# Kernel optimization log

Hardware: AMD Instinct MI355X
Metric: run time of the kernel (lower is better)

## Reference

```python
import jax, jax.numpy as jnp
import numpy as np

N, F_IN, HID, H1, E = 50000, 512, 128, 4, 800000
NEG_SLOPE = 0.2

def setup_inputs() -> dict:
    key = jax.random.key(0)
    ks = jax.random.split(key, 10)
    s = lambda fan: 1.0 / np.sqrt(fan)
    x = jax.random.normal(ks[0], (N, F_IN), jnp.float32)
    edge_index = jax.random.randint(ks[1], (2, E), 0, N, jnp.int32)
    W1 = jax.random.normal(ks[2], (F_IN, H1 * HID), jnp.float32) * s(F_IN)
    a_src1 = jax.random.normal(ks[3], (H1, HID), jnp.float32) * s(HID)
    a_dst1 = jax.random.normal(ks[4], (H1, HID), jnp.float32) * s(HID)
    b1 = jnp.zeros((H1 * HID,), jnp.float32)
    W2 = jax.random.normal(ks[5], (H1 * HID, HID), jnp.float32) * s(H1 * HID)
    a_src2 = jax.random.normal(ks[6], (1, HID), jnp.float32) * s(HID)
    a_dst2 = jax.random.normal(ks[7], (1, HID), jnp.float32) * s(HID)
    b2 = jnp.zeros((HID,), jnp.float32)
    return {"x": x, "edge_index": edge_index, "W1": W1, "a_src1": a_src1,
            "a_dst1": a_dst1, "b1": b1, "W2": W2, "a_src2": a_src2,
            "a_dst2": a_dst2, "b2": b2}

def _gat(x, src, dst, W, a_src, a_dst, b, n):
    H, C = a_src.shape
    h = (x @ W).reshape(-1, H, C)                      # [N, H, C]
    # per-edge attention logits: alpha_src[src] + alpha_dst[dst]
    e = jax.nn.leaky_relu((h * a_src).sum(-1)[src] + (h * a_dst).sum(-1)[dst],
                          NEG_SLOPE)                   # [E', H]
    # segment softmax over destination node
    m = jax.ops.segment_max(e, dst, num_segments=n)
    p = jnp.exp(e - m[dst])
    denom = jax.ops.segment_sum(p, dst, num_segments=n)
    alpha = p / (denom[dst] + 1e-16)
    # weighted scatter-add aggregation
    out = jax.ops.segment_sum(h[src] * alpha[:, :, None], dst, num_segments=n)
    return out.reshape(-1, H * C) + b

def reference(x, edge_index, W1, a_src1, a_dst1, b1, W2, a_src2, a_dst2, b2):
    loops = jnp.arange(N, dtype=edge_index.dtype)      # add_self_loops=True
    src = jnp.concatenate([edge_index[0], loops])
    dst = jnp.concatenate([edge_index[1], loops])
    h = jax.nn.elu(_gat(x, src, dst, W1, a_src1, a_dst1, b1, N))
    return _gat(h, src, dst, W2, a_src2, a_dst2, b2, N)
```

## Files before the change

kernel.cpp:

```cpp
#include <hip/hip_runtime.h>
#include <hip/hip_bf16.h>
#include <math.h>

#define NEG_SLOPE 0.2f

constexpr int N_NODES = 50000;
constexpr int F_IN    = 512;
constexpr int HID     = 128;
constexpr int H1      = 4;
constexpr int E_EDGES = 800000;
constexpr int E_TOT   = E_EDGES + N_NODES;
constexpr int DEG_CAP = 64;

typedef __attribute__((ext_vector_type(8))) short short8;
typedef __attribute__((ext_vector_type(4))) float floatx4;
typedef __attribute__((ext_vector_type(2))) float f32x2;
typedef __attribute__((ext_vector_type(4))) unsigned short ushort4v;

__device__ __forceinline__ unsigned short f2bf(float f) {
  union { float f; unsigned int u; } v; v.f = f;
  unsigned int u = v.u + 0x7FFFu + ((v.u >> 16) & 1u);
  return (unsigned short)(u >> 16);
}
__device__ __forceinline__ float bf_lo(unsigned int u) {
  union { unsigned int u; float f; } v; v.u = u << 16; return v.f;
}
__device__ __forceinline__ float bf_hi(unsigned int u) {
  union { unsigned int u; float f; } v; v.u = u & 0xFFFF0000u; return v.f;
}

__device__ __forceinline__ void store_val(float* p, float v) { *p = v; }
__device__ __forceinline__ void store_val(unsigned short* p, float v) { *p = f2bf(v); }

template <int CPT>
__device__ __forceinline__ void store_vec(unsigned short* p, const float* v) {
#pragma unroll
  for (int c = 0; c < CPT; c += 4) {
    ushort4v o;
#pragma unroll
    for (int j = 0; j < 4; ++j) o[j] = f2bf(v[c + j]);
    *(ushort4v*)(p + c) = o;
  }
}
template <int CPT>
__device__ __forceinline__ void store_vec(float* p, const float* v) {
#pragma unroll
  for (int c = 0; c < CPT; c += 4) *(float4*)(p + c) = *(const float4*)(v + c);
}

__device__ __forceinline__ void async_load16(const void* g, void* lds) {
  __builtin_amdgcn_global_load_lds(
      (const __attribute__((address_space(1))) unsigned int*)g,
      (__attribute__((address_space(3))) unsigned int*)lds, 16, 0, 0);
}

__global__ void prep_kernel(const float* __restrict__ W1, const float* __restrict__ W2,
                            unsigned short* __restrict__ W1t, unsigned short* __restrict__ W2t,
                            int* __restrict__ cnt) {
  int i = blockIdx.x * 256 + threadIdx.x;
  if (i < N_NODES) cnt[i] = 0;
  int j = i - N_NODES;
  if (j >= 0 && j < 512 * 512) {
    int n = j >> 9, k = j & 511;
    W1t[j] = f2bf(W1[k * 512 + n]);
  }
  int l = i - N_NODES - 512 * 512;
  if (l >= 0 && l < 128 * 512) {
    int n = l >> 9, k = l & 511;
    W2t[l] = f2bf(W2[k * 128 + n]);
  }
}

__global__ void fill_kernel(const int* __restrict__ ei, int* __restrict__ cnt,
                            int* __restrict__ adj) {
  int i = blockIdx.x * blockDim.x + threadIdx.x;
  if (i >= E_TOT) return;
  int s, d;
  if (i < E_EDGES) { s = ei[i]; d = ei[E_EDGES + i]; }
  else             { s = i - E_EDGES; d = s; }
  int pos = atomicAdd(&cnt[d], 1);
  if (pos < DEG_CAP) adj[d * DEG_CAP + pos] = s;
}

template <bool CVT_A, typename OT>
__global__ __launch_bounds__(256) void gemm_bf16_kernel(
    const void* __restrict__ Araw, const unsigned short* __restrict__ Bt,
    OT* __restrict__ C, const float* __restrict__ a_srcp, const float* __restrict__ a_dstp,
    float* __restrict__ alpha_src, float* __restrict__ alpha_dst,
    int M, int N, int K, int Hn, int nRowTiles) {
  __shared__ unsigned short As[128 * 32];
  __shared__ unsigned short Bs[128 * 32];
  __shared__ float red_s[128][2];
  __shared__ float red_d[128][2];

  int grp = blockIdx.x / (8 * Hn);
  int w8 = blockIdx.x % (8 * Hn);
  int head = w8 >> 3;
  int rowTile = grp * 8 + (w8 & 7);
  if (rowTile >= nRowTiles) return;
  int row0 = rowTile * 128;
  int col0 = head * 128;

  int tid = threadIdx.x;
  int lane = tid & 63, wave = tid >> 6;
  int wm = wave & 1, wn = wave >> 1;
  int l15 = lane & 15, quad = lane >> 4;

  floatx4 acc[4][4];
#pragma unroll
  for (int i = 0; i < 4; ++i)
#pragma unroll
    for (int j = 0; j < 4; ++j) acc[i][j] = (floatx4){0.f, 0.f, 0.f, 0.f};

  int seg_b = wave * 2;
  int r_in = (lane >> 2);
  int c8 = (lane & 3) * 8;

  for (int k0 = 0; k0 < K; k0 += 32) {
#pragma unroll
    for (int p = 0; p < 2; ++p) {
      int seg = seg_b + p;
      int r = seg * 16 + r_in;
      int gc = col0 + r;
      async_load16(Bt + (size_t)gc * K + k0 + c8, &Bs[seg * 512]);
    }
    if constexpr (CVT_A) {
      const float* Af = (const float*)Araw;
#pragma unroll
      for (int p = 0; p < 4; ++p) {
        int lin = tid + p * 256;
        int r = lin >> 3;
        int q = lin & 7;
        int gr = row0 + r; if (gr >= M) gr = M - 1;
        float4 f = *(const float4*)(Af + (size_t)gr * K + k0 + q * 4);
        ushort4v o;
        o[0] = f2bf(f.x); o[1] = f2bf(f.y); o[2] = f2bf(f.z); o[3] = f2bf(f.w);
        *(ushort4v*)&As[r * 32 + q * 4] = o;
      }
    } else {
      const unsigned short* Ab = (const unsigned short*)Araw;
#pragma unroll
      for (int p = 0; p < 2; ++p) {
        int seg = seg_b + p;
        int r = seg * 16 + r_in;
        int gr = row0 + r; if (gr >= M) gr = M - 1;
        async_load16(Ab + (size_t)gr * K + k0 + c8, &As[seg * 512]);
      }
    }
    __syncthreads();

    short8 a[4], b[4];
#pragma unroll
    for (int mi = 0; mi < 4; ++mi)
      a[mi] = *(const short8*)&As[(wm * 64 + mi * 16 + l15) * 32 + quad * 8];
#pragma unroll
    for (int ni = 0; ni < 4; ++ni)
      b[ni] = *(const short8*)&Bs[(wn * 64 + ni * 16 + l15) * 32 + quad * 8];
#pragma unroll
    for (int mi = 0; mi < 4; ++mi)
#pragma unroll
      for (int ni = 0; ni < 4; ++ni)
        acc[mi][ni] = __builtin_amdgcn_mfma_f32_16x16x32_bf16(a[mi], b[ni], acc[mi][ni], 0, 0, 0);
    __syncthreads();
  }

  float a_s[4], a_d[4];
#pragma unroll
  for (int ni = 0; ni < 4; ++ni) {
    int cih = wn * 64 + ni * 16 + l15;
    a_s[ni] = a_srcp[head * HID + cih];
    a_d[ni] = a_dstp[head * HID + cih];
  }

#pragma unroll
  for (int mi = 0; mi < 4; ++mi) {
#pragma unroll
    for (int r = 0; r < 4; ++r) {
      int rloc = wm * 64 + mi * 16 + quad * 4 + r;
      int grow = row0 + rloc;
      float ps = 0.f, pd = 0.f;
#pragma unroll
      for (int ni = 0; ni < 4; ++ni) {
        float v = acc[mi][ni][r];
        ps += v * a_s[ni];
        pd += v * a_d[ni];
        if (grow < M) {
          int gcol = col0 + wn * 64 + ni * 16 + l15;
          store_val(&C[(size_t)grow * N + gcol], v);
        }
      }
#pragma unroll
      for (int off = 1; off < 16; off <<= 1) {
        ps += __shfl_xor(ps, off);
        pd += __shfl_xor(pd, off);
      }
      if (l15 == 0) { red_s[rloc][wn] = ps; red_d[rloc][wn] = pd; }
    }
  }
  __syncthreads();
  if (tid < 128) {
    int grow = row0 + tid;
    if (grow < M) {
      alpha_src[(size_t)grow * Hn + head] = red_s[tid][0] + red_s[tid][1];
      alpha_dst[(size_t)grow * Hn + head] = red_d[tid][0] + red_d[tid][1];
    }
  }
}

template <int H, typename OT>
__global__ __launch_bounds__(256) void aggregate_kernel(
    const unsigned short* __restrict__ h, const float* __restrict__ asrc,
    const float* __restrict__ adst, const int* __restrict__ cnt,
    const int* __restrict__ adj, const float* __restrict__ bias,
    OT* __restrict__ out, int apply_elu, int nNodes) {
  constexpr int CPT = 8;
  constexpr int CH = H * HID;
  constexpr int NCH = CH / CPT;
  constexpr int SLOTS = 64 / NCH;
  constexpr int NW = 4;
  __shared__ float p_sh[NW][64 * H];
  __shared__ int ro_sh[NW][64];

  const int wv = threadIdx.x >> 6;
  const int lane = threadIdx.x & 63;
  const int node = blockIdx.x * NW + wv;
  if (node >= nNodes) return;
  int deg = cnt[node];
  if (deg > DEG_CAP) deg = DEG_CAP;

  int s_i = 0;
  if (lane < deg) s_i = adj[node * DEG_CAP + lane];
  float ar[H];
#pragma unroll
  for (int hh = 0; hh < H; ++hh) ar[hh] = (lane < deg) ? asrc[s_i * H + hh] : 0.f;
  ro_sh[wv][lane] = s_i * (CH * 2);
  asm volatile("s_waitcnt lgkmcnt(0)" ::: "memory");

  const int chlane = lane % NCH;
  const int slot = lane / NCH;
  const int ch = chlane * CPT;
  const int head = ch >> 7;
  const char* hb = (const char*)h + ch * 2;

  auto loadu = [&](uint4& U, int e) {
    if (e < deg) U = *(const uint4*)(hb + (unsigned)ro_sh[wv][e]);
    else         U = make_uint4(0u, 0u, 0u, 0u);
  };

  uint4 u0, u1, u2, u3, u4, u5, u6, u7;
  loadu(u0, slot);             loadu(u1, slot + SLOTS);
  loadu(u2, slot + 2 * SLOTS); loadu(u3, slot + 3 * SLOTS);
  loadu(u4, slot + 4 * SLOTS); loadu(u5, slot + 5 * SLOTS);
  loadu(u6, slot + 6 * SLOTS); loadu(u7, slot + 7 * SLOTS);

#pragma unroll
  for (int hh = 0; hh < H; ++hh) {
    float v = ar[hh] + adst[node * H + hh];
    v = (v > 0.f) ? v : NEG_SLOPE * v;
    float lg = (lane < deg) ? v : -1e30f;
#pragma unroll
    for (int o = 32; o; o >>= 1) lg = fmaxf(lg, __shfl_xor(lg, o));
    float p = (lane < deg) ? __expf(v - lg) : 0.f;
    float s = p;
#pragma unroll
    for (int o = 32; o; o >>= 1) s += __shfl_xor(s, o);
    p_sh[wv][lane * H + hh] = p * (1.f / (s + 1e-16f));
  }
  asm volatile("s_waitcnt lgkmcnt(0)" ::: "memory");

  f32x2 ac0 = {0.f, 0.f}, ac1 = {0.f, 0.f}, ac2v = {0.f, 0.f}, ac3 = {0.f, 0.f};
  auto consume = [&](const uint4& U, int e) {
    float w = p_sh[wv][(e & 63) * H + head];
    f32x2 wp = {w, w};
    f32x2 t;
    t.x = bf_lo(U.x); t.y = bf_hi(U.x); ac0  += t * wp;
    t.x = bf_lo(U.y); t.y = bf_hi(U.y); ac1  += t * wp;
    t.x = bf_lo(U.z); t.y = bf_hi(U.z); ac2v += t * wp;
    t.x = bf_lo(U.w); t.y = bf_hi(U.w); ac3  += t * wp;
  };

  int base = 0;
  for (;;) {
    int nb = base + 8 * SLOTS;
    if (nb < deg) {
      consume(u0, base + slot);             loadu(u0, nb + slot);
      consume(u1, base + slot + SLOTS);     loadu(u1, nb + slot + SLOTS);
      consume(u2, base + slot + 2 * SLOTS); loadu(u2, nb + slot + 2 * SLOTS);
      consume(u3, base + slot + 3 * SLOTS); loadu(u3, nb + slot + 3 * SLOTS);
      consume(u4, base + slot + 4 * SLOTS); loadu(u4, nb + slot + 4 * SLOTS);
      consume(u5, base + slot + 5 * SLOTS); loadu(u5, nb + slot + 5 * SLOTS);
      consume(u6, base + slot + 6 * SLOTS); loadu(u6, nb + slot + 6 * SLOTS);
      consume(u7, base + slot + 7 * SLOTS); loadu(u7, nb + slot + 7 * SLOTS);
      base = nb;
    } else {
      consume(u0, base + slot);             consume(u1, base + slot + SLOTS);
      consume(u2, base + slot + 2 * SLOTS); consume(u3, base + slot + 3 * SLOTS);
      consume(u4, base + slot + 4 * SLOTS); consume(u5, base + slot + 5 * SLOTS);
      consume(u6, base + slot + 6 * SLOTS); consume(u7, base + slot + 7 * SLOTS);
      break;
    }
  }

#pragma unroll
  for (int o = NCH; o < 64; o <<= 1) {
    ac0.x  += __shfl_xor(ac0.x, o);  ac0.y  += __shfl_xor(ac0.y, o);
    ac1.x  += __shfl_xor(ac1.x, o);  ac1.y  += __shfl_xor(ac1.y, o);
    ac2v.x += __shfl_xor(ac2v.x, o); ac2v.y += __shfl_xor(ac2v.y, o);
    ac3.x  += __shfl_xor(ac3.x, o);  ac3.y  += __shfl_xor(ac3.y, o);
  }

  if (slot == 0) {
    float r[CPT] = {ac0.x, ac0.y, ac1.x, ac1.y, ac2v.x, ac2v.y, ac3.x, ac3.y};
#pragma unroll
    for (int c = 0; c < CPT; ++c) {
      float t = r[c] + bias[ch + c];
      if (apply_elu) t = (t > 0.f) ? t : (__expf(t) - 1.f);
      r[c] = t;
    }
    store_vec<CPT>(&out[(size_t)node * CH + ch], r);
  }
}

extern "C" void kernel_launch(void* const* d_in, const int* in_sizes, int n_in,
                              void* d_out, int out_size, void* d_ws, size_t ws_size,
                              hipStream_t stream) {
  const float* x      = (const float*)d_in[0];
  const int*   ei     = (const int*)d_in[1];
  const float* W1     = (const float*)d_in[2];
  const float* a_src1 = (const float*)d_in[3];
  const float* a_dst1 = (const float*)d_in[4];
  const float* b1     = (const float*)d_in[5];
  const float* W2     = (const float*)d_in[6];
  const float* a_src2 = (const float*)d_in[7];
  const float* a_dst2 = (const float*)d_in[8];
  const float* b2     = (const float*)d_in[9];
  float* out = (float*)d_out;

  float* ws   = (float*)d_ws;
  float* as1  = ws;
  float* ad1  = as1 + N_NODES * H1;
  float* as2  = ad1 + N_NODES * H1;
  float* ad2  = as2 + N_NODES;
  unsigned short* bufA = (unsigned short*)(ad2 + N_NODES);
  unsigned short* bufB = bufA + (size_t)N_NODES * 512;
  unsigned short* hmidb = bufA;
  unsigned short* h1b   = bufB;
  unsigned short* h2b   = bufB;
  unsigned short* W1t   = bufB + (size_t)N_NODES * 512;
  unsigned short* W2t   = W1t + 512 * 512;
  int* cnt = (int*)(W2t + 128 * 512);
  int* adj = cnt + N_NODES;

  constexpr int NRT = (N_NODES + 127) / 128;
  constexpr int NRT8 = ((NRT + 7) / 8) * 8;
  constexpr int PREP_ITEMS = N_NODES + 512 * 512 + 128 * 512;

  prep_kernel<<<(PREP_ITEMS + 255) / 256, 256, 0, stream>>>(W1, W2, W1t, W2t, cnt);
  fill_kernel<<<(E_TOT + 255) / 256, 256, 0, stream>>>(ei, cnt, adj);

  gemm_bf16_kernel<true, unsigned short><<<NRT8 * H1, 256, 0, stream>>>(
      x, W1t, h1b, a_src1, a_dst1, as1, ad1, N_NODES, 512, 512, H1, NRT);
  aggregate_kernel<4, unsigned short><<<(N_NODES + 3) / 4, 256, 0, stream>>>(
      h1b, as1, ad1, cnt, adj, b1, hmidb, 1, N_NODES);

  gemm_bf16_kernel<false, unsigned short><<<NRT8, 256, 0, stream>>>(
      hmidb, W2t, h2b, a_src2, a_dst2, as2, ad2, N_NODES, 128, 512, 1, NRT);
  aggregate_kernel<1, float><<<(N_NODES + 3) / 4, 256, 0, stream>>>(
      h2b, as2, ad2, cnt, adj, b2, out, 0, N_NODES);
}
```

Baseline: 492.4 us.

## Fuse adjacency fill into first GEMM launch and use one-wave aggregate blocks

The edge-fill atomics are moved into extra blocks of the first GEMM launch, so the fill and the GEMM run in one grid and one kernel launch plus its serialization is removed. The aggregate kernel now uses 64-thread blocks with one node per block, which simplifies shared-memory indexing and removes the bounds check. For layer 1 it also loads the per-source attention scalars as one float4. The risk is that the fill blocks compete with the GEMM blocks for resources, and tiny blocks may limit occupancy or add scheduling overhead.

```diff
diff --git a/kernel.cpp b/kernel.cpp
--- a/kernel.cpp
+++ b/kernel.cpp
@@ -71,27 +71,30 @@
   }
 }
 
-__global__ void fill_kernel(const int* __restrict__ ei, int* __restrict__ cnt,
-                            int* __restrict__ adj) {
-  int i = blockIdx.x * blockDim.x + threadIdx.x;
-  if (i >= E_TOT) return;
-  int s, d;
-  if (i < E_EDGES) { s = ei[i]; d = ei[E_EDGES + i]; }
-  else             { s = i - E_EDGES; d = s; }
-  int pos = atomicAdd(&cnt[d], 1);
-  if (pos < DEG_CAP) adj[d * DEG_CAP + pos] = s;
-}
-
-template <bool CVT_A, typename OT>
+template <bool CVT_A, bool FILL, typename OT>
 __global__ __launch_bounds__(256) void gemm_bf16_kernel(
     const void* __restrict__ Araw, const unsigned short* __restrict__ Bt,
     OT* __restrict__ C, const float* __restrict__ a_srcp, const float* __restrict__ a_dstp,
     float* __restrict__ alpha_src, float* __restrict__ alpha_dst,
-    int M, int N, int K, int Hn, int nRowTiles) {
+    int M, int N, int K, int Hn, int nRowTiles,
+    const int* __restrict__ ei, int* __restrict__ cnt, int* __restrict__ adj,
+    int gemmBlocks) {
   __shared__ unsigned short As[128 * 32];
   __shared__ unsigned short Bs[128 * 32];
   __shared__ float red_s[128][2];
   __shared__ float red_d[128][2];
+
+  if (FILL && blockIdx.x >= gemmBlocks) {
+    int i = (blockIdx.x - gemmBlocks) * 256 + threadIdx.x;
+    if (i < E_TOT) {
+      int s, d;
+      if (i < E_EDGES) { s = ei[i]; d = ei[E_EDGES + i]; }
+      else             { s = i - E_EDGES; d = s; }
+      int pos = atomicAdd(&cnt[d], 1);
+      if (pos < DEG_CAP) adj[d * DEG_CAP + pos] = s;
+    }
+    return;
+  }
 
   int grp = blockIdx.x / (8 * Hn);
   int w8 = blockIdx.x % (8 * Hn);
@@ -208,32 +211,34 @@
 }
 
 template <int H, typename OT>
-__global__ __launch_bounds__(256) void aggregate_kernel(
+__global__ __launch_bounds__(64) void aggregate_kernel(
     const unsigned short* __restrict__ h, const float* __restrict__ asrc,
     const float* __restrict__ adst, const int* __restrict__ cnt,
     const int* __restrict__ adj, const float* __restrict__ bias,
-    OT* __restrict__ out, int apply_elu, int nNodes) {
+    OT* __restrict__ out, int apply_elu) {
   constexpr int CPT = 8;
   constexpr int CH = H * HID;
   constexpr int NCH = CH / CPT;
   constexpr int SLOTS = 64 / NCH;
-  constexpr int NW = 4;
-  __shared__ float p_sh[NW][64 * H];
-  __shared__ int ro_sh[NW][64];
-
-  const int wv = threadIdx.x >> 6;
-  const int lane = threadIdx.x & 63;
-  const int node = blockIdx.x * NW + wv;
-  if (node >= nNodes) return;
+  __shared__ float p_sh[64 * H];
+  __shared__ int ro_sh[64];
+
+  const int node = blockIdx.x;
+  const int lane = threadIdx.x;
   int deg = cnt[node];
   if (deg > DEG_CAP) deg = DEG_CAP;
 
   int s_i = 0;
   if (lane < deg) s_i = adj[node * DEG_CAP + lane];
+  ro_sh[lane] = s_i * (CH * 2);
   float ar[H];
-#pragma unroll
-  for (int hh = 0; hh < H; ++hh) ar[hh] = (lane < deg) ? asrc[s_i * H + hh] : 0.f;
-  ro_sh[wv][lane] = s_i * (CH * 2);
+  if constexpr (H == 4) {
+    float4 f = (lane < deg) ? *(const float4*)(asrc + (size_t)s_i * 4)
+                            : make_float4(0.f, 0.f, 0.f, 0.f);
+    ar[0] = f.x; ar[1] = f.y; ar[2] = f.z; ar[3] = f.w;
+  } else {
+    ar[0] = (lane < deg) ? asrc[s_i] : 0.f;
+  }
   asm volatile("s_waitcnt lgkmcnt(0)" ::: "memory");
 
   const int chlane = lane % NCH;
@@ -243,7 +248,7 @@
   const char* hb = (const char*)h + ch * 2;
 
   auto loadu = [&](uint4& U, int e) {
-    if (e < deg) U = *(const uint4*)(hb + (unsigned)ro_sh[wv][e]);
+    if (e < deg) U = *(const uint4*)(hb + (unsigned)ro_sh[e]);
     else         U = make_uint4(0u, 0u, 0u, 0u);
   };
 
@@ -264,13 +269,13 @@
     float s = p;
 #pragma unroll
     for (int o = 32; o; o >>= 1) s += __shfl_xor(s, o);
-    p_sh[wv][lane * H + hh] = p * (1.f / (s + 1e-16f));
+    p_sh[lane * H + hh] = p * (1.f / (s + 1e-16f));
   }
   asm volatile("s_waitcnt lgkmcnt(0)" ::: "memory");
 
   f32x2 ac0 = {0.f, 0.f}, ac1 = {0.f, 0.f}, ac2v = {0.f, 0.f}, ac3 = {0.f, 0.f};
   auto consume = [&](const uint4& U, int e) {
-    float w = p_sh[wv][(e & 63) * H + head];
+    float w = p_sh[(e & 63) * H + head];
     f32x2 wp = {w, w};
     f32x2 t;
     t.x = bf_lo(U.x); t.y = bf_hi(U.x); ac0  += t * wp;
@@ -354,17 +359,21 @@
   constexpr int NRT = (N_NODES + 127) / 128;
   constexpr int NRT8 = ((NRT + 7) / 8) * 8;
   constexpr int PREP_ITEMS = N_NODES + 512 * 512 + 128 * 512;
+  constexpr int FILL_BLOCKS = (E_TOT + 255) / 256;
+  constexpr int GEMM1_BLOCKS = NRT8 * H1;
 
   prep_kernel<<<(PREP_ITEMS + 255) / 256, 256, 0, stream>>>(W1, W2, W1t, W2t, cnt);
-  fill_kernel<<<(E_TOT + 255) / 256, 256, 0, stream>>>(ei, cnt, adj);
-
-  gemm_bf16_kernel<true, unsigned short><<<NRT8 * H1, 256, 0, stream>>>(
-      x, W1t, h1b, a_src1, a_dst1, as1, ad1, N_NODES, 512, 512, H1, NRT);
-  aggregate_kernel<4, unsigned short><<<(N_NODES + 3) / 4, 256, 0, stream>>>(
-      h1b, as1, ad1, cnt, adj, b1, hmidb, 1, N_NODES);
-
-  gemm_bf16_kernel<false, unsigned short><<<NRT8, 256, 0, stream>>>(
-      hmidb, W2t, h2b, a_src2, a_dst2, as2, ad2, N_NODES, 128, 512, 1, NRT);
-  aggregate_kernel<1, float><<<(N_NODES + 3) / 4, 256, 0, stream>>>(
-      h2b, as2, ad2, cnt, adj, b2, out, 0, N_NODES);
-}
+
+  gemm_bf16_kernel<true, true, unsigned short>
+      <<<GEMM1_BLOCKS + FILL_BLOCKS, 256, 0, stream>>>(
+      x, W1t, h1b, a_src1, a_dst1, as1, ad1, N_NODES, 512, 512, H1, NRT,
+      ei, cnt, adj, GEMM1_BLOCKS);
+  aggregate_kernel<4, unsigned short><<<N_NODES, 64, 0, stream>>>(
+      h1b, as1, ad1, cnt, adj, b1, hmidb, 1);
+
+  gemm_bf16_kernel<false, false, unsigned short><<<NRT8, 256, 0, stream>>>(
+      hmidb, W2t, h2b, a_src2, a_dst2, as2, ad2, N_NODES, 128, 512, 1, NRT,
+      nullptr, nullptr, nullptr, 0);
+  aggregate_kernel<1, float><<<N_NODES, 64, 0, stream>>>(
+      h2b, as2, ad2, cnt, adj, b2, out, 0);
+}
```

After: 467.1 us. 1.05x faster.
